# Performance work log

Measured on AMD Instinct MI355X. Metric: run time of the kernel, lower is better.

The kernel has to match this reference:

```python
import jax, jax.numpy as jnp
import numpy as np

B, K, P, T = 4096, 128, 64, 4

def setup_inputs() -> dict:
    key = jax.random.key(0)
    ks = jax.random.split(key, 9)
    s = lambda k, shp: jax.random.normal(k, shp, dtype=jnp.float32) * 0.1
    return {
        "x": jax.random.normal(ks[0], (B, K, 1), dtype=jnp.float32),
        "w": jax.random.normal(ks[1], (B, K, 1), dtype=jnp.float32),
        "W1": s(ks[2], (P, 1)),   # theta_1: 1 -> p
        "W2": s(ks[3], (P, P)),   # theta_2: p -> p
        "W3": s(ks[4], (P, P)),   # theta_3: p -> p
        "W4": s(ks[5], (P, 1)),   # theta_4: 1 -> p
        "W5": s(ks[6], (1, 2 * P)),  # theta_5: 2p -> 1
        "W6": s(ks[7], (P, P)),   # theta_6: p -> p
        "W7": s(ks[8], (P, P)),   # theta_7: p -> p
    }


def reference(x, w, W1, W2, W3, W4, W5, W6, W7):
    # x, w: (B, K, 1). torch Linear(in,out,bias=False): y = v @ W.T, W: (out,in)
    b, k, _ = x.shape
    p = W1.shape[0]
    # per-node feature messages (invariant across T iterations in original code)
    tmsg = jax.nn.relu(jnp.einsum('bki,pi->bkp', w, W4))   # relu(theta_4(w_k)), (B,K,p)
    sum_t = tmsg.sum(axis=1, keepdims=True)                # (B,1,p)
    xmsg = jnp.einsum('bki,pi->bkp', x, W1)                # theta_1(x_k), (B,K,p)
    mu = jnp.zeros((b, k, p), dtype=x.dtype)
    for _ in range(T):
        sum_mu = mu.sum(axis=1, keepdims=True)             # (B,1,p)
        mu = jax.nn.relu(
            xmsg
            + jnp.einsum('bkp,qp->bkq', sum_mu - mu, W2)   # theta_2(sum_mu - mu_k)
            + jnp.einsum('bkp,qp->bkq', sum_t - tmsg, W3)  # theta_3(sum_t - t_k)
        )
    pooled = jax.nn.relu(jnp.einsum('bp,qp->bq', mu.sum(axis=1), W6))  # (B,p)
    local = jnp.einsum('bkp,qp->bkq', mu, W7)                           # (B,K,p)
    # theta_5(concat(relu(theta_6(pool)), theta_7(mu_k))); split W5 = [W5a | W5b]
    W5a, W5b = W5[:, :p], W5[:, p:]
    q = jnp.einsum('bp,op->bo', pooled, W5a)[:, None, :] + jnp.einsum('bkp,op->bko', local, W5b)
    return q  # (B, K, 1)
```

## Files before the change

kernel.cpp:

```cpp
#include <hip/hip_runtime.h>

typedef __bf16 bf16;
typedef __bf16 bf16x4 __attribute__((ext_vector_type(4)));
typedef __bf16 bf16x8 __attribute__((ext_vector_type(8)));
typedef float  f32x2  __attribute__((ext_vector_type(2)));
typedef float  f32x4  __attribute__((ext_vector_type(4)));

#define MFMA16(a, b, c) __builtin_amdgcn_mfma_f32_16x16x32_bf16((a), (b), (c), 0, 0, 0)


template<int CTRL>
__device__ __forceinline__ float dpp_add(float v) {
    int t = __builtin_amdgcn_update_dpp(0, __float_as_int(v), CTRL, 0xF, 0xF, false);
    return v + __int_as_float(t);
}

__device__ __forceinline__ void bfly16(f32x2* s) {
#pragma unroll
    for (int i = 0; i < 8; ++i) { s[i][0] = dpp_add<0x121>(s[i][0]); s[i][1] = dpp_add<0x121>(s[i][1]); }
#pragma unroll
    for (int i = 0; i < 8; ++i) { s[i][0] = dpp_add<0x122>(s[i][0]); s[i][1] = dpp_add<0x122>(s[i][1]); }
#pragma unroll
    for (int i = 0; i < 8; ++i) { s[i][0] = dpp_add<0x124>(s[i][0]); s[i][1] = dpp_add<0x124>(s[i][1]); }
#pragma unroll
    for (int i = 0; i < 8; ++i) { s[i][0] = dpp_add<0x128>(s[i][0]); s[i][1] = dpp_add<0x128>(s[i][1]); }
}

__device__ __forceinline__ f32x2 fma2(f32x2 a, f32x2 b, f32x2 c) {
    return __builtin_elementwise_fma(a, b, c);
}
__device__ __forceinline__ f32x2 max2(f32x2 a, f32x2 b) {
    return __builtin_elementwise_max(a, b);
}

__global__ __launch_bounds__(64, 2)
void qnet_kernel(const float* __restrict__ Xg, const float* __restrict__ Wg,
                 const float* __restrict__ W1g, const float* __restrict__ W2g,
                 const float* __restrict__ W3g, const float* __restrict__ W4g,
                 const float* __restrict__ W5g, const float* __restrict__ W6g,
                 const float* __restrict__ W7g, float* __restrict__ Outg)
{
    __shared__ __align__(16) bf16 muS[128 * 64];
    __shared__ __align__(16) float uS[64];
    __shared__ __align__(16) float smS[64];

    const int lane = threadIdx.x;
    const int b    = blockIdx.x;
    const int l15  = lane & 15;
    const int quad = lane >> 4;
    const int sw   = l15 & 7;

    float xv0 = Xg[b * 128 + lane], xv1 = Xg[b * 128 + 64 + lane];
    float wv0 = Wg[b * 128 + lane], wv1 = Wg[b * 128 + 64 + lane];

    float Ap = fmaxf(wv0, 0.f) + fmaxf(wv1, 0.f);
    float Bn = fmaxf(-wv0, 0.f) + fmaxf(-wv1, 0.f);
#pragma unroll
    for (int m = 1; m < 64; m <<= 1) { Ap += __shfl_xor(Ap, m); Bn += __shfl_xor(Bn, m); }

    float sp = 0.f, sm = 0.f;
#pragma unroll
    for (int c = 0; c < 16; ++c) {
        f32x4 w4 = *(const f32x4*)&W4g[c * 4];
        f32x4 w3 = *(const f32x4*)&W3g[lane * 64 + c * 4];
#pragma unroll
        for (int e = 0; e < 4; ++e) {
            sp += fmaxf(w4[e], 0.f) * w3[e];
            sm += fmaxf(-w4[e], 0.f) * w3[e];
        }
    }
    f32x2 w1P[4][2], v3pP[4][2], v3mP[4][2];
#pragma unroll
    for (int qt = 0; qt < 4; ++qt) {
        f32x4 w1v = *(const f32x4*)&W1g[qt * 16 + quad * 4];
#pragma unroll
        for (int e = 0; e < 4; ++e) {
            const int q = qt * 16 + quad * 4 + e;
            v3pP[qt][e >> 1][e & 1] = __shfl(sp, q);
            v3mP[qt][e >> 1][e & 1] = __shfl(sm, q);
            w1P[qt][e >> 1][e & 1]  = w1v[e];
        }
    }

    {
        float u = 0.f;
#pragma unroll
        for (int c = 0; c < 16; ++c) {
            f32x4 w5v = *(const f32x4*)&W5g[64 + c * 4];
#pragma unroll
            for (int e = 0; e < 4; ++e) u += w5v[e] * W7g[(c * 4 + e) * 64 + lane];
        }
        uS[lane] = u;
    }

    bf16x8 w2h[4][2];
#pragma unroll
    for (int qt = 0; qt < 4; ++qt)
#pragma unroll
        for (int s = 0; s < 2; ++s) {
            const float* src = &W2g[(qt * 16 + l15) * 64 + s * 32 + quad * 8];
            f32x4 f0 = *(const f32x4*)src;
            f32x4 f1 = *(const f32x4*)(src + 4);
            bf16x8 h;
#pragma unroll
            for (int e = 0; e < 4; ++e) { h[e] = (bf16)f0[e]; h[4 + e] = (bf16)f1[e]; }
            w2h[qt][s] = h;
        }

    const f32x2 zz = {0.f, 0.f};

    f32x2 smv2[8];
#pragma unroll
    for (int i = 0; i < 8; ++i) smv2[i] = zz;
#pragma unroll
    for (int kt = 0; kt < 8; ++kt) {
        const int src = (kt & 3) * 16 + l15;
        float xs_ = __shfl((kt < 4) ? xv0 : xv1, src);
        float ws_ = __shfl((kt < 4) ? wv0 : wv1, src);
        f32x2 xs2 = {xs_, xs_};
        float ap_ = Ap - fmaxf(ws_, 0.f);
        float bn_ = Bn - fmaxf(-ws_, 0.f);
        f32x2 ap2 = {ap_, ap_}, bn2 = {bn_, bn_};
        const int row = (kt * 16 + l15) * 64;
#pragma unroll
        for (int qt = 0; qt < 4; ++qt) {
            f32x2 t01 = fma2(ap2, v3pP[qt][0], bn2 * v3mP[qt][0]);
            t01 = fma2(xs2, w1P[qt][0], t01);
            f32x2 v01 = max2(t01, zz);
            f32x2 t23 = fma2(ap2, v3pP[qt][1], bn2 * v3mP[qt][1]);
            t23 = fma2(xs2, w1P[qt][1], t23);
            f32x2 v23 = max2(t23, zz);
            smv2[qt * 2]     += v01;
            smv2[qt * 2 + 1] += v23;
            bf16x4 h = {(bf16)v01[0], (bf16)v01[1], (bf16)v23[0], (bf16)v23[1]};
            *(bf16x4*)&muS[row + ((2 * qt + (quad >> 1)) ^ sw) * 8 + 4 * (quad & 1)] = h;
        }
    }

    const f32x4 zero4 = {0.f, 0.f, 0.f, 0.f};
    for (int it = 0; it < 3; ++it) {
        bfly16(smv2);
        if (l15 == 0) {
#pragma unroll
            for (int qt = 0; qt < 4; ++qt) {
                f32x4 v = {smv2[qt * 2][0], smv2[qt * 2][1],
                           smv2[qt * 2 + 1][0], smv2[qt * 2 + 1][1]};
                *(f32x4*)&smS[qt * 16 + quad * 4] = v;
            }
        }
        bf16x8 bh0, bl0, bh1, bl1;
        {
            f32x4 pA = *(const f32x4*)&smS[quad * 8];
            f32x4 pB = *(const f32x4*)&smS[quad * 8 + 4];
#pragma unroll
            for (int e = 0; e < 4; ++e) {
                bf16 h = (bf16)pA[e]; bh0[e] = h;     bl0[e] = (bf16)(pA[e] - (float)h);
                bf16 g = (bf16)pB[e]; bh0[4 + e] = g; bl0[4 + e] = (bf16)(pB[e] - (float)g);
            }
            pA = *(const f32x4*)&smS[32 + quad * 8];
            pB = *(const f32x4*)&smS[32 + quad * 8 + 4];
#pragma unroll
            for (int e = 0; e < 4; ++e) {
                bf16 h = (bf16)pA[e]; bh1[e] = h;     bl1[e] = (bf16)(pA[e] - (float)h);
                bf16 g = (bf16)pB[e]; bh1[4 + e] = g; bl1[4 + e] = (bf16)(pB[e] - (float)g);
            }
        }
        f32x2 s2p[4][2];
#pragma unroll
        for (int qt = 0; qt < 4; ++qt) {
            f32x4 a = MFMA16(w2h[qt][0], bh0, zero4);
            a = MFMA16(w2h[qt][1], bh1, a);
            a = MFMA16(w2h[qt][0], bl0, a);
            a = MFMA16(w2h[qt][1], bl1, a);
            s2p[qt][0] = __builtin_shufflevector(a, a, 0, 1);
            s2p[qt][1] = __builtin_shufflevector(a, a, 2, 3);
        }

#pragma unroll
        for (int i = 0; i < 8; ++i) smv2[i] = zz;
#pragma unroll
        for (int kt = 0; kt < 8; ++kt) {
            const int src = (kt & 3) * 16 + l15;
            float xs_ = __shfl((kt < 4) ? xv0 : xv1, src);
            float ws_ = __shfl((kt < 4) ? wv0 : wv1, src);
            f32x2 xs2 = {xs_, xs_};
            float ap_ = Ap - fmaxf(ws_, 0.f);
            float bn_ = Bn - fmaxf(-ws_, 0.f);
            f32x2 ap2 = {ap_, ap_}, bn2 = {bn_, bn_};
            const int row = (kt * 16 + l15) * 64;
            bf16x8 m0 = *(const bf16x8*)&muS[row + ((quad) ^ sw) * 8];
            bf16x8 m1 = *(const bf16x8*)&muS[row + ((4 + quad) ^ sw) * 8];
#pragma unroll
            for (int qt = 0; qt < 4; ++qt) {
                f32x4 a = MFMA16(w2h[qt][0], m0, zero4);
                a = MFMA16(w2h[qt][1], m1, a);
                f32x2 a01 = __builtin_shufflevector(a, a, 0, 1);
                f32x2 a23 = __builtin_shufflevector(a, a, 2, 3);
                f32x2 t01 = fma2(xs2, w1P[qt][0], s2p[qt][0]);
                t01 = fma2(ap2, v3pP[qt][0], t01);
                t01 = fma2(bn2, v3mP[qt][0], t01);
                f32x2 v01 = max2(t01 - a01, zz);
                f32x2 t23 = fma2(xs2, w1P[qt][1], s2p[qt][1]);
                t23 = fma2(ap2, v3pP[qt][1], t23);
                t23 = fma2(bn2, v3mP[qt][1], t23);
                f32x2 v23 = max2(t23 - a23, zz);
                smv2[qt * 2]     += v01;
                smv2[qt * 2 + 1] += v23;
                bf16x4 h = {(bf16)v01[0], (bf16)v01[1], (bf16)v23[0], (bf16)v23[1]};
                *(bf16x4*)&muS[row + ((2 * qt + (quad >> 1)) ^ sw) * 8 + 4 * (quad & 1)] = h;
            }
        }
    }

    bfly16(smv2);
    if (l15 == 0) {
#pragma unroll
        for (int qt = 0; qt < 4; ++qt) {
            f32x4 v = {smv2[qt * 2][0], smv2[qt * 2][1],
                       smv2[qt * 2 + 1][0], smv2[qt * 2 + 1][1]};
            *(f32x4*)&smS[qt * 16 + quad * 4] = v;
        }
    }

    float pl = 0.f;
#pragma unroll
    for (int c = 0; c < 16; ++c) {
        f32x4 sv = *(const f32x4*)&smS[c * 4];
        f32x4 w6 = *(const f32x4*)&W6g[lane * 64 + c * 4];
#pragma unroll
        for (int e = 0; e < 4; ++e) pl = fmaf(sv[e], w6[e], pl);
    }
    float qa = fmaxf(pl, 0.f) * W5g[lane];
#pragma unroll
    for (int m = 1; m < 64; m <<= 1) qa += __shfl_xor(qa, m);

    f32x4 uf[2][2];
#pragma unroll
    for (int s = 0; s < 2; ++s) {
        uf[s][0] = *(const f32x4*)&uS[s * 32 + quad * 8];
        uf[s][1] = *(const f32x4*)&uS[s * 32 + quad * 8 + 4];
    }

    float res[8];
#pragma unroll
    for (int kt = 0; kt < 8; ++kt) {
        const int row = (kt * 16 + l15) * 64;
        bf16x8 m0 = *(const bf16x8*)&muS[row + ((quad) ^ sw) * 8];
        bf16x8 m1 = *(const bf16x8*)&muS[row + ((4 + quad) ^ sw) * 8];
        float r = 0.f;
#pragma unroll
        for (int j = 0; j < 4; ++j) {
            r = fmaf((float)m0[j],     uf[0][0][j], r);
            r = fmaf((float)m0[4 + j], uf[0][1][j], r);
            r = fmaf((float)m1[j],     uf[1][0][j], r);
            r = fmaf((float)m1[4 + j], uf[1][1][j], r);
        }
        r += __shfl_xor(r, 16); r += __shfl_xor(r, 32);
        res[kt] = r;
    }
    float rA0 = (quad & 1) ? res[1] : res[0];
    float rA1 = (quad & 1) ? res[3] : res[2];
    float rA  = (quad & 2) ? rA1 : rA0;
    float rB0 = (quad & 1) ? res[5] : res[4];
    float rB1 = (quad & 1) ? res[7] : res[6];
    float rB  = (quad & 2) ? rB1 : rB0;
    Outg[b * 128 + lane]      = qa + rA;
    Outg[b * 128 + 64 + lane] = qa + rB;
}

extern "C" void kernel_launch(void* const* d_in, const int* in_sizes, int n_in,
                              void* d_out, int out_size, void* d_ws, size_t ws_size,
                              hipStream_t stream) {
    (void)n_in; (void)d_ws; (void)ws_size; (void)out_size;
    const int B = in_sizes[0] >> 7;
    qnet_kernel<<<B, 64, 0, stream>>>(
        (const float*)d_in[0], (const float*)d_in[1], (const float*)d_in[2],
        (const float*)d_in[3], (const float*)d_in[4], (const float*)d_in[5],
        (const float*)d_in[6], (const float*)d_in[7], (const float*)d_in[8],
        (float*)d_out);
}
```

Baseline: 115.9 us.

## Process two batch items per block to amortize weight setup

Each single-wave block now handles two batch elements in sequence, so the per-block weight preprocessing (W2 conversion to bf16 into registers, W1/W3/W4 folding, u vector) is done once for two items. Per-item x/w values are now loaded straight into the lane layout used by the k-loops, which removes the per-tile shuffles, and the Ap/Bn sums use a 16-lane DPP row reduction instead of a full-wave shuffle reduction. Halving the grid to 2048 blocks of one wave each lowers parallelism and makes each block's work serial. It also assumes an even batch size. Shared-memory reuse across the two items relies on in-wave ordering, with no barrier.

```diff
diff --git a/kernel.cpp b/kernel.cpp
--- a/kernel.cpp
+++ b/kernel.cpp
@@ -13,6 +13,12 @@
 __device__ __forceinline__ float dpp_add(float v) {
     int t = __builtin_amdgcn_update_dpp(0, __float_as_int(v), CTRL, 0xF, 0xF, false);
     return v + __int_as_float(t);
+}
+
+__device__ __forceinline__ float row_sum16(float v) {
+    v = dpp_add<0x121>(v); v = dpp_add<0x122>(v);
+    v = dpp_add<0x124>(v); v = dpp_add<0x128>(v);
+    return v;
 }
 
 __device__ __forceinline__ void bfly16(f32x2* s) {
@@ -45,18 +51,9 @@
     __shared__ __align__(16) float smS[64];
 
     const int lane = threadIdx.x;
-    const int b    = blockIdx.x;
     const int l15  = lane & 15;
     const int quad = lane >> 4;
     const int sw   = l15 & 7;
-
-    float xv0 = Xg[b * 128 + lane], xv1 = Xg[b * 128 + 64 + lane];
-    float wv0 = Wg[b * 128 + lane], wv1 = Wg[b * 128 + 64 + lane];
-
-    float Ap = fmaxf(wv0, 0.f) + fmaxf(wv1, 0.f);
-    float Bn = fmaxf(-wv0, 0.f) + fmaxf(-wv1, 0.f);
-#pragma unroll
-    for (int m = 1; m < 64; m <<= 1) { Ap += __shfl_xor(Ap, m); Bn += __shfl_xor(Bn, m); }
 
     float sp = 0.f, sm = 0.f;
 #pragma unroll
@@ -108,37 +105,124 @@
         }
 
     const f32x2 zz = {0.f, 0.f};
-
-    f32x2 smv2[8];
-#pragma unroll
-    for (int i = 0; i < 8; ++i) smv2[i] = zz;
-#pragma unroll
-    for (int kt = 0; kt < 8; ++kt) {
-        const int src = (kt & 3) * 16 + l15;
-        float xs_ = __shfl((kt < 4) ? xv0 : xv1, src);
-        float ws_ = __shfl((kt < 4) ? wv0 : wv1, src);
-        f32x2 xs2 = {xs_, xs_};
-        float ap_ = Ap - fmaxf(ws_, 0.f);
-        float bn_ = Bn - fmaxf(-ws_, 0.f);
-        f32x2 ap2 = {ap_, ap_}, bn2 = {bn_, bn_};
-        const int row = (kt * 16 + l15) * 64;
-#pragma unroll
-        for (int qt = 0; qt < 4; ++qt) {
-            f32x2 t01 = fma2(ap2, v3pP[qt][0], bn2 * v3mP[qt][0]);
-            t01 = fma2(xs2, w1P[qt][0], t01);
-            f32x2 v01 = max2(t01, zz);
-            f32x2 t23 = fma2(ap2, v3pP[qt][1], bn2 * v3mP[qt][1]);
-            t23 = fma2(xs2, w1P[qt][1], t23);
-            f32x2 v23 = max2(t23, zz);
-            smv2[qt * 2]     += v01;
-            smv2[qt * 2 + 1] += v23;
-            bf16x4 h = {(bf16)v01[0], (bf16)v01[1], (bf16)v23[0], (bf16)v23[1]};
-            *(bf16x4*)&muS[row + ((2 * qt + (quad >> 1)) ^ sw) * 8 + 4 * (quad & 1)] = h;
-        }
-    }
-
     const f32x4 zero4 = {0.f, 0.f, 0.f, 0.f};
-    for (int it = 0; it < 3; ++it) {
+
+#pragma unroll 1
+    for (int bi = 0; bi < 2; ++bi) {
+        const int b = blockIdx.x * 2 + bi;
+
+        float xs[8], ws[8];
+#pragma unroll
+        for (int kt = 0; kt < 8; ++kt) {
+            const int k = ((kt >> 2) << 6) + ((kt & 3) << 4) + l15;
+            xs[kt] = Xg[b * 128 + k];
+            ws[kt] = Wg[b * 128 + k];
+        }
+        float apl = 0.f, bnl = 0.f;
+#pragma unroll
+        for (int kt = 0; kt < 8; ++kt) {
+            apl += fmaxf(ws[kt], 0.f);
+            bnl += fmaxf(-ws[kt], 0.f);
+        }
+        const float Ap = row_sum16(apl);
+        const float Bn = row_sum16(bnl);
+
+        f32x2 smv2[8];
+#pragma unroll
+        for (int i = 0; i < 8; ++i) smv2[i] = zz;
+#pragma unroll
+        for (int kt = 0; kt < 8; ++kt) {
+            f32x2 xs2 = {xs[kt], xs[kt]};
+            float ap_ = Ap - fmaxf(ws[kt], 0.f);
+            float bn_ = Bn - fmaxf(-ws[kt], 0.f);
+            f32x2 ap2 = {ap_, ap_}, bn2 = {bn_, bn_};
+            const int row = (kt * 16 + l15) * 64;
+#pragma unroll
+            for (int qt = 0; qt < 4; ++qt) {
+                f32x2 t01 = fma2(ap2, v3pP[qt][0], bn2 * v3mP[qt][0]);
+                t01 = fma2(xs2, w1P[qt][0], t01);
+                f32x2 v01 = max2(t01, zz);
+                f32x2 t23 = fma2(ap2, v3pP[qt][1], bn2 * v3mP[qt][1]);
+                t23 = fma2(xs2, w1P[qt][1], t23);
+                f32x2 v23 = max2(t23, zz);
+                smv2[qt * 2]     += v01;
+                smv2[qt * 2 + 1] += v23;
+                bf16x4 h = {(bf16)v01[0], (bf16)v01[1], (bf16)v23[0], (bf16)v23[1]};
+                *(bf16x4*)&muS[row + ((2 * qt + (quad >> 1)) ^ sw) * 8 + 4 * (quad & 1)] = h;
+            }
+        }
+
+        for (int it = 0; it < 3; ++it) {
+            bfly16(smv2);
+            if (l15 == 0) {
+#pragma unroll
+                for (int qt = 0; qt < 4; ++qt) {
+                    f32x4 v = {smv2[qt * 2][0], smv2[qt * 2][1],
+                               smv2[qt * 2 + 1][0], smv2[qt * 2 + 1][1]};
+                    *(f32x4*)&smS[qt * 16 + quad * 4] = v;
+                }
+            }
+            bf16x8 bh0, bl0, bh1, bl1;
+            {
+                f32x4 pA = *(const f32x4*)&smS[quad * 8];
+                f32x4 pB = *(const f32x4*)&smS[quad * 8 + 4];
+#pragma unroll
+                for (int e = 0; e < 4; ++e) {
+                    bf16 h = (bf16)pA[e]; bh0[e] = h;     bl0[e] = (bf16)(pA[e] - (float)h);
+                    bf16 g = (bf16)pB[e]; bh0[4 + e] = g; bl0[4 + e] = (bf16)(pB[e] - (float)g);
+                }
+                pA = *(const f32x4*)&smS[32 + quad * 8];
+                pB = *(const f32x4*)&smS[32 + quad * 8 + 4];
+#pragma unroll
+                for (int e = 0; e < 4; ++e) {
+                    bf16 h = (bf16)pA[e]; bh1[e] = h;     bl1[e] = (bf16)(pA[e] - (float)h);
+                    bf16 g = (bf16)pB[e]; bh1[4 + e] = g; bl1[4 + e] = (bf16)(pB[e] - (float)g);
+                }
+            }
+            f32x2 s2p[4][2];
+#pragma unroll
+            for (int qt = 0; qt < 4; ++qt) {
+                f32x4 a = MFMA16(w2h[qt][0], bh0, zero4);
+                a = MFMA16(w2h[qt][1], bh1, a);
+                a = MFMA16(w2h[qt][0], bl0, a);
+                a = MFMA16(w2h[qt][1], bl1, a);
+                s2p[qt][0] = __builtin_shufflevector(a, a, 0, 1);
+                s2p[qt][1] = __builtin_shufflevector(a, a, 2, 3);
+            }
+
+#pragma unroll
+            for (int i = 0; i < 8; ++i) smv2[i] = zz;
+#pragma unroll
+            for (int kt = 0; kt < 8; ++kt) {
+                f32x2 xs2 = {xs[kt], xs[kt]};
+                float ap_ = Ap - fmaxf(ws[kt], 0.f);
+                float bn_ = Bn - fmaxf(-ws[kt], 0.f);
+                f32x2 ap2 = {ap_, ap_}, bn2 = {bn_, bn_};
+                const int row = (kt * 16 + l15) * 64;
+                bf16x8 m0 = *(const bf16x8*)&muS[row + ((quad) ^ sw) * 8];
+                bf16x8 m1 = *(const bf16x8*)&muS[row + ((4 + quad) ^ sw) * 8];
+#pragma unroll
+                for (int qt = 0; qt < 4; ++qt) {
+                    f32x4 a = MFMA16(w2h[qt][0], m0, zero4);
+                    a = MFMA16(w2h[qt][1], m1, a);
+                    f32x2 a01 = __builtin_shufflevector(a, a, 0, 1);
+                    f32x2 a23 = __builtin_shufflevector(a, a, 2, 3);
+                    f32x2 t01 = fma2(xs2, w1P[qt][0], s2p[qt][0]);
+                    t01 = fma2(ap2, v3pP[qt][0], t01);
+                    t01 = fma2(bn2, v3mP[qt][0], t01);
+                    f32x2 v01 = max2(t01 - a01, zz);
+                    f32x2 t23 = fma2(xs2, w1P[qt][1], s2p[qt][1]);
+                    t23 = fma2(ap2, v3pP[qt][1], t23);
+                    t23 = fma2(bn2, v3mP[qt][1], t23);
+                    f32x2 v23 = max2(t23 - a23, zz);
+                    smv2[qt * 2]     += v01;
+                    smv2[qt * 2 + 1] += v23;
+                    bf16x4 h = {(bf16)v01[0], (bf16)v01[1], (bf16)v23[0], (bf16)v23[1]};
+                    *(bf16x4*)&muS[row + ((2 * qt + (quad >> 1)) ^ sw) * 8 + 4 * (quad & 1)] = h;
+                }
+            }
+        }
+
         bfly16(smv2);
         if (l15 == 0) {
 #pragma unroll
@@ -148,124 +232,52 @@
                 *(f32x4*)&smS[qt * 16 + quad * 4] = v;
             }
         }
-        bf16x8 bh0, bl0, bh1, bl1;
-        {
-            f32x4 pA = *(const f32x4*)&smS[quad * 8];
-            f32x4 pB = *(const f32x4*)&smS[quad * 8 + 4];
-#pragma unroll
-            for (int e = 0; e < 4; ++e) {
-                bf16 h = (bf16)pA[e]; bh0[e] = h;     bl0[e] = (bf16)(pA[e] - (float)h);
-                bf16 g = (bf16)pB[e]; bh0[4 + e] = g; bl0[4 + e] = (bf16)(pB[e] - (float)g);
-            }
-            pA = *(const f32x4*)&smS[32 + quad * 8];
-            pB = *(const f32x4*)&smS[32 + quad * 8 + 4];
-#pragma unroll
-            for (int e = 0; e < 4; ++e) {
-                bf16 h = (bf16)pA[e]; bh1[e] = h;     bl1[e] = (bf16)(pA[e] - (float)h);
-                bf16 g = (bf16)pB[e]; bh1[4 + e] = g; bl1[4 + e] = (bf16)(pB[e] - (float)g);
-            }
-        }
-        f32x2 s2p[4][2];
-#pragma unroll
-        for (int qt = 0; qt < 4; ++qt) {
-            f32x4 a = MFMA16(w2h[qt][0], bh0, zero4);
-            a = MFMA16(w2h[qt][1], bh1, a);
-            a = MFMA16(w2h[qt][0], bl0, a);
-            a = MFMA16(w2h[qt][1], bl1, a);
-            s2p[qt][0] = __builtin_shufflevector(a, a, 0, 1);
-            s2p[qt][1] = __builtin_shufflevector(a, a, 2, 3);
-        }
-
-#pragma unroll
-        for (int i = 0; i < 8; ++i) smv2[i] = zz;
-#pragma unroll
-        for (int kt = 0; kt < 8; ++kt) {
-            const int src = (kt & 3) * 16 + l15;
-            float xs_ = __shfl((kt < 4) ? xv0 : xv1, src);
-            float ws_ = __shfl((kt < 4) ? wv0 : wv1, src);
-            f32x2 xs2 = {xs_, xs_};
-            float ap_ = Ap - fmaxf(ws_, 0.f);
-            float bn_ = Bn - fmaxf(-ws_, 0.f);
-            f32x2 ap2 = {ap_, ap_}, bn2 = {bn_, bn_};
+
+        float pl = 0.f;
+#pragma unroll
+        for (int c = 0; c < 16; ++c) {
+            f32x4 sv = *(const f32x4*)&smS[c * 4];
+            f32x4 w6 = *(const f32x4*)&W6g[lane * 64 + c * 4];
+#pragma unroll
+            for (int e = 0; e < 4; ++e) pl = fmaf(sv[e], w6[e], pl);
+        }
+        float qa = fmaxf(pl, 0.f) * W5g[lane];
+#pragma unroll
+        for (int m = 1; m < 64; m <<= 1) qa += __shfl_xor(qa, m);
+
+        f32x4 uf[2][2];
+#pragma unroll
+        for (int s = 0; s < 2; ++s) {
+            uf[s][0] = *(const f32x4*)&uS[s * 32 + quad * 8];
+            uf[s][1] = *(const f32x4*)&uS[s * 32 + quad * 8 + 4];
+        }
+
+        float res[8];
+#pragma unroll
+        for (int kt = 0; kt < 8; ++kt) {
             const int row = (kt * 16 + l15) * 64;
             bf16x8 m0 = *(const bf16x8*)&muS[row + ((quad) ^ sw) * 8];
             bf16x8 m1 = *(const bf16x8*)&muS[row + ((4 + quad) ^ sw) * 8];
-#pragma unroll
-            for (int qt = 0; qt < 4; ++qt) {
-                f32x4 a = MFMA16(w2h[qt][0], m0, zero4);
-                a = MFMA16(w2h[qt][1], m1, a);
-                f32x2 a01 = __builtin_shufflevector(a, a, 0, 1);
-                f32x2 a23 = __builtin_shufflevector(a, a, 2, 3);
-                f32x2 t01 = fma2(xs2, w1P[qt][0], s2p[qt][0]);
-                t01 = fma2(ap2, v3pP[qt][0], t01);
-                t01 = fma2(bn2, v3mP[qt][0], t01);
-                f32x2 v01 = max2(t01 - a01, zz);
-                f32x2 t23 = fma2(xs2, w1P[qt][1], s2p[qt][1]);
-                t23 = fma2(ap2, v3pP[qt][1], t23);
-                t23 = fma2(bn2, v3mP[qt][1], t23);
-                f32x2 v23 = max2(t23 - a23, zz);
-                smv2[qt * 2]     += v01;
-                smv2[qt * 2 + 1] += v23;
-                bf16x4 h = {(bf16)v01[0], (bf16)v01[1], (bf16)v23[0], (bf16)v23[1]};
-                *(bf16x4*)&muS[row + ((2 * qt + (quad >> 1)) ^ sw) * 8 + 4 * (quad & 1)] = h;
-            }
-        }
-    }
-
-    bfly16(smv2);
-    if (l15 == 0) {
-#pragma unroll
-        for (int qt = 0; qt < 4; ++qt) {
-            f32x4 v = {smv2[qt * 2][0], smv2[qt * 2][1],
-                       smv2[qt * 2 + 1][0], smv2[qt * 2 + 1][1]};
-            *(f32x4*)&smS[qt * 16 + quad * 4] = v;
-        }
-    }
-
-    float pl = 0.f;
-#pragma unroll
-    for (int c = 0; c < 16; ++c) {
-        f32x4 sv = *(const f32x4*)&smS[c * 4];
-        f32x4 w6 = *(const f32x4*)&W6g[lane * 64 + c * 4];
-#pragma unroll
-        for (int e = 0; e < 4; ++e) pl = fmaf(sv[e], w6[e], pl);
-    }
-    float qa = fmaxf(pl, 0.f) * W5g[lane];
-#pragma unroll
-    for (int m = 1; m < 64; m <<= 1) qa += __shfl_xor(qa, m);
-
-    f32x4 uf[2][2];
-#pragma unroll
-    for (int s = 0; s < 2; ++s) {
-        uf[s][0] = *(const f32x4*)&uS[s * 32 + quad * 8];
-        uf[s][1] = *(const f32x4*)&uS[s * 32 + quad * 8 + 4];
-    }
-
-    float res[8];
-#pragma unroll
-    for (int kt = 0; kt < 8; ++kt) {
-        const int row = (kt * 16 + l15) * 64;
-        bf16x8 m0 = *(const bf16x8*)&muS[row + ((quad) ^ sw) * 8];
-        bf16x8 m1 = *(const bf16x8*)&muS[row + ((4 + quad) ^ sw) * 8];
-        float r = 0.f;
-#pragma unroll
-        for (int j = 0; j < 4; ++j) {
-            r = fmaf((float)m0[j],     uf[0][0][j], r);
-            r = fmaf((float)m0[4 + j], uf[0][1][j], r);
-            r = fmaf((float)m1[j],     uf[1][0][j], r);
-            r = fmaf((float)m1[4 + j], uf[1][1][j], r);
-        }
-        r += __shfl_xor(r, 16); r += __shfl_xor(r, 32);
-        res[kt] = r;
-    }
-    float rA0 = (quad & 1) ? res[1] : res[0];
-    float rA1 = (quad & 1) ? res[3] : res[2];
-    float rA  = (quad & 2) ? rA1 : rA0;
-    float rB0 = (quad & 1) ? res[5] : res[4];
-    float rB1 = (quad & 1) ? res[7] : res[6];
-    float rB  = (quad & 2) ? rB1 : rB0;
-    Outg[b * 128 + lane]      = qa + rA;
-    Outg[b * 128 + 64 + lane] = qa + rB;
+            float r = 0.f;
+#pragma unroll
+            for (int j = 0; j < 4; ++j) {
+                r = fmaf((float)m0[j],     uf[0][0][j], r);
+                r = fmaf((float)m0[4 + j], uf[0][1][j], r);
+                r = fmaf((float)m1[j],     uf[1][0][j], r);
+                r = fmaf((float)m1[4 + j], uf[1][1][j], r);
+            }
+            r += __shfl_xor(r, 16); r += __shfl_xor(r, 32);
+            res[kt] = r;
+        }
+        float rA0 = (quad & 1) ? res[1] : res[0];
+        float rA1 = (quad & 1) ? res[3] : res[2];
+        float rA  = (quad & 2) ? rA1 : rA0;
+        float rB0 = (quad & 1) ? res[5] : res[4];
+        float rB1 = (quad & 1) ? res[7] : res[6];
+        float rB  = (quad & 2) ? rB1 : rB0;
+        Outg[b * 128 + lane]      = qa + rA;
+        Outg[b * 128 + 64 + lane] = qa + rB;
+    }
 }
 
 extern "C" void kernel_launch(void* const* d_in, const int* in_sizes, int n_in,
@@ -273,7 +285,7 @@
                               hipStream_t stream) {
     (void)n_in; (void)d_ws; (void)ws_size; (void)out_size;
     const int B = in_sizes[0] >> 7;
-    qnet_kernel<<<B, 64, 0, stream>>>(
+    qnet_kernel<<<B / 2, 64, 0, stream>>>(
         (const float*)d_in[0], (const float*)d_in[1], (const float*)d_in[2],
         (const float*)d_in[3], (const float*)d_in[4], (const float*)d_in[5],
         (const float*)d_in[6], (const float*)d_in[7], (const float*)d_in[8],
```

Result: no change. 117.8 us (+1.7%).
